# Optimization experiments

Hardware: AMD Instinct MI355X
Metric: run time of the kernel (lower is better)

The kernel has to match this reference:

```python
import jax, jax.numpy as jnp
import numpy as np

N_EXAMPLES = 10  # hardcoded repeat_interleave(10) in the source

def setup_inputs() -> dict:
    key = jax.random.key(0)
    k1, k2, k3, k4 = jax.random.split(key, 4)
    B, L, S, H = 8, 256, 512, 1024
    return {
        "output": jax.random.normal(k1, (B * N_EXAMPLES, L, H), dtype=jnp.float32),
        "context0": jax.random.normal(k2, (B * N_EXAMPLES, L, H), dtype=jnp.float32),
        "context1": jax.random.normal(k3, (B, S, H), dtype=jnp.float32),
        "mask": jnp.zeros((B * N_EXAMPLES, L), dtype=bool),
        "W_out": jax.random.normal(k4, (H, 3 * H), dtype=jnp.float32) * 0.02,
        "b_out": jnp.zeros((H,), dtype=jnp.float32),
    }

def reference(output, context0, context1, mask, W_out, b_out):
    # output, context0: [B*10, L, H]; context1: [B, S, H]
    # NOTE: in the torch source, `attn.data.masked_fill(mask, -inf)` is NOT
    # in-place and its result is discarded, so the mask has no effect on the
    # math. We reproduce that faithfully: `mask` is unused.
    del mask
    set_ctx = jnp.repeat(context1, N_EXAMPLES, axis=0)  # [B*10, S, H]
    # example-attention branch: bmm -> softmax -> bmm
    ex_attn = jax.nn.softmax(jnp.einsum('bld,bsd->bls', output, context0), axis=-1)  # [B*10, L, L]
    # set-attention branch: bmm -> softmax -> bmm
    set_attn = jax.nn.softmax(jnp.einsum('bld,bsd->bls', output, set_ctx), axis=-1)  # [B*10, L, S]
    ex_c = jnp.einsum('bls,bsd->bld', ex_attn, context0)   # [B*10, L, H]
    set_c = jnp.einsum('bls,bsd->bld', set_attn, set_ctx)  # [B*10, L, H]
    all_info = jnp.concatenate([output, ex_c, set_c], axis=-1)  # [B*10, L, 3H]
    out = jnp.tanh(jnp.einsum('blk,hk->blh', all_info, W_out) + b_out)  # [B*10, L, H]
    return (out, ex_attn, set_attn)
```

## Files before the change

### kernel.cpp

```cpp
#include <hip/hip_runtime.h>
#include <stdint.h>
#include <math.h>

typedef unsigned short u16;
typedef __attribute__((ext_vector_type(8))) short short8;
typedef __attribute__((ext_vector_type(4))) float floatx4;

__device__ __forceinline__ u16 f32_to_bf16(float f) {
    union { float f; uint32_t u; } v; v.f = f;
    uint32_t r = v.u + 0x7FFF + ((v.u >> 16) & 1);
    return (u16)(r >> 16);
}
__device__ __forceinline__ float bf16_to_f32(u16 h) {
    union { uint32_t u; float f; } v; v.u = ((uint32_t)h) << 16; return v.f;
}

__device__ __forceinline__ void gl_lds16(const u16* g, u16* l) {
    __builtin_amdgcn_global_load_lds(
        (const __attribute__((address_space(1))) void*)g,
        (__attribute__((address_space(3))) void*)l, 16, 0, 0);
}


__global__ void split_kernel(const float4* __restrict__ x, ushort4* __restrict__ hi,
                             ushort4* __restrict__ lo, long n4) {
    long i = (long)blockIdx.x * blockDim.x + threadIdx.x;
    if (i >= n4) return;
    float4 v = x[i];
    ushort4 h, l;
    h.x = f32_to_bf16(v.x); l.x = f32_to_bf16(v.x - bf16_to_f32(h.x));
    h.y = f32_to_bf16(v.y); l.y = f32_to_bf16(v.y - bf16_to_f32(h.y));
    h.z = f32_to_bf16(v.z); l.z = f32_to_bf16(v.z - bf16_to_f32(h.z));
    h.w = f32_to_bf16(v.w); l.w = f32_to_bf16(v.w - bf16_to_f32(h.w));
    hi[i] = h; lo[i] = l;
}

__global__ void conv_kernel(const float4* __restrict__ x, ushort4* __restrict__ hi, long n4) {
    long i = (long)blockIdx.x * blockDim.x + threadIdx.x;
    if (i >= n4) return;
    float4 v = x[i];
    ushort4 h;
    h.x = f32_to_bf16(v.x); h.y = f32_to_bf16(v.y);
    h.z = f32_to_bf16(v.z); h.w = f32_to_bf16(v.w);
    hi[i] = h;
}

__global__ void transpose_u16(const u16* __restrict__ src, u16* __restrict__ dst,
                              int R, int C) {
    __shared__ u16 tile[32][34];
    long base = (long)blockIdx.z * R * C;
    int c0 = blockIdx.x * 32, r0 = blockIdx.y * 32;
    #pragma unroll
    for (int i = threadIdx.y; i < 32; i += 8)
        tile[i][threadIdx.x] = src[base + (long)(r0 + i) * C + c0 + threadIdx.x];
    __syncthreads();
    #pragma unroll
    for (int i = threadIdx.y; i < 32; i += 8)
        dst[base + (long)(c0 + i) * R + r0 + threadIdx.x] = tile[threadIdx.x][i];
}

template <int VPT>
__global__ void softmax_rows(float* __restrict__ data, u16* __restrict__ outb) {
    int row = blockIdx.x * 4 + (threadIdx.x >> 6);
    int lane = threadIdx.x & 63;
    long base = (long)row * (VPT * 64) + lane;
    float v[VPT];
    #pragma unroll
    for (int i = 0; i < VPT; ++i) v[i] = data[base + i * 64];
    float m = v[0];
    #pragma unroll
    for (int i = 1; i < VPT; ++i) m = fmaxf(m, v[i]);
    #pragma unroll
    for (int off = 32; off > 0; off >>= 1) m = fmaxf(m, __shfl_xor(m, off, 64));
    float s = 0.f;
    #pragma unroll
    for (int i = 0; i < VPT; ++i) { v[i] = __expf(v[i] - m); s += v[i]; }
    #pragma unroll
    for (int off = 32; off > 0; off >>= 1) s += __shfl_xor(s, off, 64);
    float inv = 1.0f / s;
    #pragma unroll
    for (int i = 0; i < VPT; ++i) {
        float r = v[i] * inv;
        data[base + i * 64] = r;
        outb[base + i * 64] = f32_to_bf16(r);
    }
}

struct GemmP {
    const u16* A[3];
    const u16* B[3];
    const u16* B2[3];
    long strideAb, strideBb, strideB2b, strideCb, strideC2b;
    int bdiv, bdiv2, nseg, Kper, kshift, kmask, nt, lda, ldb, ldb2, ldc, ldc2, mode;
    int gx, gy, nx1;
    float* Cf; float* Cf2; u16* Cb; const float* bias;
};

__global__ __launch_bounds__(256) void gemm_bt(GemmP p) {
    __shared__ u16 As[128 * 64];
    __shared__ u16 Bs[128 * 64];
    const int tid  = threadIdx.x;
    const int lane = tid & 63;
    const int wave = tid >> 6;
    const int quad = lane >> 4;
    const int l15  = lane & 15;
    const int wm = (wave & 1) * 64;
    const int wn = (wave >> 1) * 64;

    const int f  = blockIdx.x;
    const int Tx = gridDim.x >> 3;
    const int t  = (f & 7) * Tx + (f >> 3);
    const int n  = t % p.gx;
    const int r  = t / p.gx;
    const int m0 = (r % p.gy) * 128;
    const int bz = r / p.gy;

    const u16* Bsegs[3];
    int ldb, ldc, nn, bdv;
    long bstr, cstr;
    float* Cf;
    if (n < p.nx1) {
        Bsegs[0] = p.B[0]; Bsegs[1] = p.B[1]; Bsegs[2] = p.B[2];
        ldb = p.ldb; ldc = p.ldc; bstr = p.strideBb; cstr = p.strideCb;
        Cf = p.Cf; bdv = p.bdiv; nn = n;
    } else {
        Bsegs[0] = p.B2[0]; Bsegs[1] = p.B2[1]; Bsegs[2] = p.B2[2];
        ldb = p.ldb2; ldc = p.ldc2; bstr = p.strideB2b; cstr = p.strideC2b;
        Cf = p.Cf2; bdv = p.bdiv2; nn = n - p.nx1;
    }
    const int n0 = nn * 128;

    const int stg_r8 = tid >> 3;
    const int stg_c  = ((tid & 7) ^ (stg_r8 & 7)) * 8;
    const int xorl   = l15 & 7;

    floatx4 acc[4][4];
    #pragma unroll
    for (int i = 0; i < 4; ++i)
        #pragma unroll
        for (int j = 0; j < 4; ++j)
            acc[i][j] = (floatx4){0.f, 0.f, 0.f, 0.f};

    const long aoff = (long)bz * p.strideAb + (long)m0 * p.lda;
    const long boff = (long)(bz / bdv) * bstr + (long)n0 * ldb;

    for (int seg = 0; seg < p.nseg; ++seg) {
        const u16* Ag = p.A[seg] + aoff;
        const u16* Bg = Bsegs[seg] + boff;
        for (int k0 = 0; k0 < p.Kper; k0 += 64) {
            __syncthreads();
            #pragma unroll
            for (int i = 0; i < 4; ++i) {
                const int rr = i * 32 + stg_r8;
                gl_lds16(Ag + (long)rr * p.lda + k0 + stg_c, &As[(i * 256 + tid) * 8]);
            }
            #pragma unroll
            for (int i = 0; i < 4; ++i) {
                const int rr = i * 32 + stg_r8;
                gl_lds16(Bg + (long)rr * ldb + k0 + stg_c, &Bs[(i * 256 + tid) * 8]);
            }
            __syncthreads();
            #pragma unroll
            for (int kk = 0; kk < 2; ++kk) {
                const int cs = ((kk * 4 + quad) ^ xorl) * 8;
                short8 af[4], bfr[4];
                #pragma unroll
                for (int i = 0; i < 4; ++i)
                    af[i] = *(const short8*)&As[(wm + i * 16 + l15) * 64 + cs];
                #pragma unroll
                for (int i = 0; i < 4; ++i)
                    bfr[i] = *(const short8*)&Bs[(wn + i * 16 + l15) * 64 + cs];
                #pragma unroll
                for (int mi = 0; mi < 4; ++mi)
                    #pragma unroll
                    for (int ni = 0; ni < 4; ++ni)
                        acc[mi][ni] = __builtin_amdgcn_mfma_f32_16x16x32_bf16(
                            af[mi], bfr[ni], acc[mi][ni], 0, 0, 0);
            }
        }
    }

    const long coff = (long)bz * cstr;
    const int rb = m0 + wm + quad * 4;
    const int cbase = n0 + wn + l15;
    if (p.mode == 2) {
        #pragma unroll
        for (int ni = 0; ni < 4; ++ni) {
            const float bv = p.bias[cbase + ni * 16];
            #pragma unroll
            for (int mi = 0; mi < 4; ++mi)
                #pragma unroll
                for (int j = 0; j < 4; ++j)
                    Cf[coff + (long)(rb + mi * 16 + j) * ldc + cbase + ni * 16] =
                        tanhf(acc[mi][ni][j] + bv);
        }
    } else if (p.mode == 0) {
        #pragma unroll
        for (int ni = 0; ni < 4; ++ni)
            #pragma unroll
            for (int mi = 0; mi < 4; ++mi)
                #pragma unroll
                for (int j = 0; j < 4; ++j)
                    Cf[coff + (long)(rb + mi * 16 + j) * ldc + cbase + ni * 16] =
                        acc[mi][ni][j];
    } else {
        #pragma unroll
        for (int ni = 0; ni < 4; ++ni)
            #pragma unroll
            for (int mi = 0; mi < 4; ++mi)
                #pragma unroll
                for (int j = 0; j < 4; ++j)
                    p.Cb[coff + (long)(rb + mi * 16 + j) * ldc + cbase + ni * 16] =
                        f32_to_bf16(acc[mi][ni][j]);
    }
}

__global__ __launch_bounds__(512, 2) void gemm_bt8(GemmP p) {
    __shared__ u16 As[32768];
    __shared__ u16 Bs[32768];
    const int tid  = threadIdx.x;
    const int lane = tid & 63;
    const int wave = tid >> 6;
    const int quad = lane >> 4;
    const int l15  = lane & 15;
    const int wr   = wave >> 2;
    const int wc   = wave & 3;

    const int f  = blockIdx.x;
    const int Tx = gridDim.x >> 3;
    const int t  = (f & 7) * Tx + (f >> 3);
    const int n  = t % p.gx;
    const int r  = t / p.gx;
    const int m0 = (r % p.gy) * 256;
    const int bz = r / p.gy;

    const u16 *B0, *B1, *B2p;
    int ldb, ldc, nn, bdv;
    long bstr, cstr;
    float* Cf;
    if (n < p.nx1) {
        B0 = p.B[0]; B1 = p.B[1]; B2p = p.B[2];
        ldb = p.ldb; ldc = p.ldc; bstr = p.strideBb; cstr = p.strideCb;
        Cf = p.Cf; bdv = p.bdiv; nn = n;
    } else {
        B0 = p.B2[0]; B1 = p.B2[1]; B2p = p.B2[2];
        ldb = p.ldb2; ldc = p.ldc2; bstr = p.strideB2b; cstr = p.strideC2b;
        Cf = p.Cf2; bdv = p.bdiv2; nn = n - p.nx1;
    }
    const int n0 = nn * 256;

    const long aoff = (long)bz * p.strideAb + (long)m0 * p.lda;
    const long boff = (long)(bz / bdv) * bstr + (long)n0 * ldb;

    const int srow = tid >> 2;
    const int sgc  = ((tid & 3) ^ ((srow >> 1) & 3)) * 8;

    const u16* a0 = p.A[0] + aoff + (long)srow * p.lda + sgc;
    const u16* a1 = p.A[1] + aoff + (long)srow * p.lda + sgc;
    const u16* a2 = p.A[2] + aoff + (long)srow * p.lda + sgc;
    const u16* b0 = B0 + boff + (long)srow * ldb + sgc;
    const u16* b1 = B1 + boff + (long)srow * ldb + sgc;
    const u16* b2 = B2p + boff + (long)srow * ldb + sgc;
    const long aStep128 = (long)128 * p.lda;
    const long bStep128 = (long)128 * ldb;

    const int rA = wr * 128 + l15;
    const u16* pA = As + rA * 32 + ((quad ^ ((rA >> 1) & 3)) * 8);
    const int rB = wc * 64 + l15;
    const u16* pB = Bs + rB * 32 + ((quad ^ ((rB >> 1) & 3)) * 8);

    const int nt = p.nt;

    auto stA = [&](int kt, int kk) {
        if (kt < nt) {
            const int seg = kt >> p.kshift;
            const u16* base = (seg == 0) ? a0 : ((seg == 1) ? a1 : a2);
            const u16* g = base + (((kt & p.kmask) << 6) + kk * 32);
            u16* d = &As[((((kt & 1) << 1) | kk) << 13) + tid * 8];
            gl_lds16(g, d);
            gl_lds16(g + aStep128, d + 4096);
        }
    };
    auto stB = [&](int kt, int kk) {
        if (kt < nt) {
            const int seg = kt >> p.kshift;
            const u16* base = (seg == 0) ? b0 : ((seg == 1) ? b1 : b2);
            const u16* g = base + (((kt & p.kmask) << 6) + kk * 32);
            u16* d = &Bs[((((kt & 1) << 1) | kk) << 13) + tid * 8];
            gl_lds16(g, d);
            gl_lds16(g + bStep128, d + 4096);
        }
    };

    floatx4 acc[8][4];
    #pragma unroll
    for (int i = 0; i < 8; ++i)
        #pragma unroll
        for (int j = 0; j < 4; ++j)
            acc[i][j] = (floatx4){0.f, 0.f, 0.f, 0.f};

    stA(0, 0); stB(0, 0); stA(0, 1); stB(0, 1); stA(1, 0); stB(1, 0);
    asm volatile("s_waitcnt vmcnt(4)" ::: "memory");
    __builtin_amdgcn_s_barrier();

    short8 af[4], bf[4];

#define QPHASE(SO, MH, LOADB, STAGE)                                        \
    {                                                                       \
        _Pragma("unroll")                                                   \
        for (int mi = 0; mi < 4; ++mi)                                      \
            af[mi] = *(const short8*)(pA + (SO) + (MH) * 2048 + mi * 512);  \
        if (LOADB) {                                                        \
            _Pragma("unroll")                                               \
            for (int ni = 0; ni < 4; ++ni)                                  \
                bf[ni] = *(const short8*)(pB + (SO) + ni * 512);            \
        }                                                                   \
        STAGE;                                                              \
        __builtin_amdgcn_s_barrier();                                       \
        asm volatile("s_waitcnt lgkmcnt(0)" ::: "memory");                  \
        __builtin_amdgcn_sched_barrier(0);                                  \
        __builtin_amdgcn_s_setprio(1);                                      \
        _Pragma("unroll")                                                   \
        for (int mi = 0; mi < 4; ++mi)                                      \
            _Pragma("unroll")                                               \
            for (int ni = 0; ni < 4; ++ni)                                  \
                acc[(MH) * 4 + mi][ni] =                                    \
                    __builtin_amdgcn_mfma_f32_16x16x32_bf16(                \
                        af[mi], bf[ni], acc[(MH) * 4 + mi][ni], 0, 0, 0);   \
        __builtin_amdgcn_s_setprio(0);                                      \
        __builtin_amdgcn_sched_barrier(0);                                  \
    }

    for (int kt = 0; kt < nt; ++kt) {
        const int so0 = (kt & 1) << 14;
        const int so1 = so0 + 8192;
        QPHASE(so0, 0, true,  stA(kt + 1, 1));
        __builtin_amdgcn_s_barrier();
        QPHASE(so0, 1, false, stB(kt + 1, 1));
        __builtin_amdgcn_s_barrier();
        QPHASE(so1, 0, true,  stA(kt + 2, 0));
        __builtin_amdgcn_s_barrier();
        QPHASE(so1, 1, false, stB(kt + 2, 0));
        if (kt + 2 < nt) {
            asm volatile("s_waitcnt vmcnt(4)" ::: "memory");
        } else {
            asm volatile("s_waitcnt vmcnt(0)" ::: "memory");
        }
        __builtin_amdgcn_s_barrier();
    }
#undef QPHASE

    const long coff = (long)bz * cstr;
    const int rb = m0 + wr * 128 + quad * 4;
    const int cb = n0 + wc * 64 + l15;
    if (p.mode == 2) {
        #pragma unroll
        for (int ni = 0; ni < 4; ++ni) {
            const float bv = p.bias[cb + ni * 16];
            #pragma unroll
            for (int mi = 0; mi < 8; ++mi)
                #pragma unroll
                for (int j = 0; j < 4; ++j)
                    Cf[coff + (long)(rb + mi * 16 + j) * ldc + cb + ni * 16] =
                        tanhf(acc[mi][ni][j] + bv);
        }
    } else if (p.mode == 0) {
        #pragma unroll
        for (int ni = 0; ni < 4; ++ni)
            #pragma unroll
            for (int mi = 0; mi < 8; ++mi)
                #pragma unroll
                for (int j = 0; j < 4; ++j)
                    Cf[coff + (long)(rb + mi * 16 + j) * ldc + cb + ni * 16] =
                        acc[mi][ni][j];
    } else {
        #pragma unroll
        for (int ni = 0; ni < 4; ++ni)
            #pragma unroll
            for (int mi = 0; mi < 8; ++mi)
                #pragma unroll
                for (int j = 0; j < 4; ++j)
                    p.Cb[coff + (long)(rb + mi * 16 + j) * ldc + cb + ni * 16] =
                        f32_to_bf16(acc[mi][ni][j]);
    }
}

extern "C" void kernel_launch(void* const* d_in, const int* in_sizes, int n_in,
                              void* d_out, int out_size, void* d_ws, size_t ws_size,
                              hipStream_t stream) {
    const int BT = 80, L = 256, S = 512, H = 1024;
    const long NO    = (long)BT * L * H;
    const long NC1   = (long)8 * S * H;
    const long NW    = (long)H * 3 * H;
    const long NEXA  = (long)BT * L * L;
    const long NSETA = (long)BT * L * S;

    const float* X    = (const float*)d_in[0];
    const float* C0   = (const float*)d_in[1];
    const float* C1   = (const float*)d_in[2];
    const float* Wf   = (const float*)d_in[4];
    const float* bias = (const float*)d_in[5];

    float* out  = (float*)d_out;
    float* exa  = out + NO;
    float* seta = exa + NEXA;

    char* wsb = (char*)d_ws;
    size_t off = 0;
    auto alloc = [&](long nbytes) -> void* {
        void* p = (void*)(wsb + off);
        off += ((size_t)nbytes + 255) & ~(size_t)255;
        return p;
    };
    u16* Xhi  = (u16*)alloc(NO * 2);
    u16* Xlo  = (u16*)alloc(NO * 2);
    u16* C0hi = (u16*)alloc(NO * 2);
    u16* C0lo = (u16*)alloc(NO * 2);
    u16* C1hi = (u16*)alloc(NC1 * 2);
    u16* C1lo = (u16*)alloc(NC1 * 2);
    u16* Wb   = (u16*)alloc(NW * 2);
    u16* exab = (u16*)alloc(NEXA * 2);
    u16* setab= (u16*)alloc(NSETA * 2);
    u16* C0T = C0lo;
    u16* C1T = C1lo;
    u16* exc = Xlo;
    u16* setc = C0hi;

    split_kernel<<<(int)(NO / 4 / 256), 256, 0, stream>>>((const float4*)X, (ushort4*)Xhi, (ushort4*)Xlo, NO / 4);
    split_kernel<<<(int)(NO / 4 / 256), 256, 0, stream>>>((const float4*)C0, (ushort4*)C0hi, (ushort4*)C0lo, NO / 4);
    split_kernel<<<(int)(NC1 / 4 / 256), 256, 0, stream>>>((const float4*)C1, (ushort4*)C1hi, (ushort4*)C1lo, NC1 / 4);
    conv_kernel<<<(int)(NW / 4 / 256), 256, 0, stream>>>((const float4*)Wf, (ushort4*)Wb, NW / 4);

    {
        GemmP p{};
        p.A[0] = Xhi;  p.A[1] = Xlo;  p.A[2] = Xhi;
        p.B[0]  = C0hi; p.B[1]  = C0hi; p.B[2]  = C0lo;
        p.B2[0] = C1hi; p.B2[1] = C1hi; p.B2[2] = C1lo;
        p.strideAb = (long)L * H;
        p.strideBb = (long)L * H;  p.strideB2b = (long)S * H;
        p.strideCb = (long)L * L;  p.strideC2b = (long)L * S;
        p.bdiv = 1; p.bdiv2 = 10;
        p.nseg = 3; p.Kper = H; p.lda = H; p.ldb = H; p.ldb2 = H;
        p.ldc = L; p.ldc2 = S; p.mode = 0;
        p.gx = 6; p.gy = 2; p.nx1 = 2;
        p.Cf = exa; p.Cf2 = seta;
        gemm_bt<<<dim3(6 * 2 * BT, 1, 1), 256, 0, stream>>>(p);
    }
    softmax_rows<4><<<BT * L / 4, 256, 0, stream>>>(exa, exab);
    softmax_rows<8><<<BT * L / 4, 256, 0, stream>>>(seta, setab);

    transpose_u16<<<dim3(H / 32, L / 32, BT), dim3(32, 8), 0, stream>>>(C0hi, C0T, L, H);
    transpose_u16<<<dim3(H / 32, S / 32, 8), dim3(32, 8), 0, stream>>>(C1hi, C1T, S, H);

    {
        GemmP p{};
        p.A[0] = exab; p.B[0] = C0T;
        p.strideAb = (long)L * L; p.strideBb = (long)H * L; p.strideCb = (long)L * H;
        p.bdiv = 1; p.kshift = 2; p.kmask = 3; p.nt = 4;
        p.lda = L; p.ldb = L; p.ldc = H; p.mode = 1;
        p.gx = 4; p.gy = 1; p.nx1 = 4;
        p.Cb = exc;
        gemm_bt8<<<dim3(4 * 1 * BT, 1, 1), 512, 0, stream>>>(p);
    }
    {
        GemmP p{};
        p.A[0] = setab; p.B[0] = C1T;
        p.strideAb = (long)L * S; p.strideBb = (long)H * S; p.strideCb = (long)L * H;
        p.bdiv = 10; p.kshift = 3; p.kmask = 7; p.nt = 8;
        p.lda = S; p.ldb = S; p.ldc = H; p.mode = 1;
        p.gx = 4; p.gy = 1; p.nx1 = 4;
        p.Cb = setc;
        gemm_bt8<<<dim3(4 * 1 * BT, 1, 1), 512, 0, stream>>>(p);
    }
    {
        GemmP p{};
        p.A[0] = Xhi; p.A[1] = exc; p.A[2] = setc;
        p.B[0] = Wb;  p.B[1] = Wb + 1024; p.B[2] = Wb + 2048;
        p.strideAb = 0; p.strideBb = 0; p.strideCb = 0;
        p.bdiv = 1; p.nseg = 3; p.Kper = H; p.lda = H; p.ldb = 3 * H; p.ldc = H; p.mode = 2;
        p.gx = 8; p.gy = BT * L / 128; p.nx1 = 8;
        p.Cf = out; p.bias = bias;
        gemm_bt<<<dim3(8 * (BT * L / 128), 1, 1), 256, 0, stream>>>(p);
    }
}
```

Baseline: 865.7 us.

## Run attention-score GEMM on 256x256 pipelined gemm_bt8 kernel with segment-generic B pointers

The first GEMM (scores for both the example and set branches, using a three-segment split-bf16 K loop) moves from the 128x128 single-buffered gemm_bt kernel to the 256x256, 8-wave, double-buffered gemm_bt8 kernel. gemm_bt8 now reads B through the n-dependent Bsegs array, so one launch can serve both output targets, and it computes segment pointers inline instead of precomputing six base pointers. The larger tiles give more data reuse and the staged loads give more overlap, in exchange for fewer blocks (240 instead of 960) and some extra address arithmetic per stage.

```diff
diff --git a/kernel.cpp b/kernel.cpp
--- a/kernel.cpp
+++ b/kernel.cpp
@@ -96,23 +96,23 @@
     float* Cf; float* Cf2; u16* Cb; const float* bias;
 };
 
-__global__ __launch_bounds__(256) void gemm_bt(GemmP p) {
-    __shared__ u16 As[128 * 64];
-    __shared__ u16 Bs[128 * 64];
+__global__ __launch_bounds__(512, 2) void gemm_bt8(GemmP p) {
+    __shared__ u16 As[32768];
+    __shared__ u16 Bs[32768];
     const int tid  = threadIdx.x;
     const int lane = tid & 63;
     const int wave = tid >> 6;
     const int quad = lane >> 4;
     const int l15  = lane & 15;
-    const int wm = (wave & 1) * 64;
-    const int wn = (wave >> 1) * 64;
+    const int wr   = wave >> 2;
+    const int wc   = wave & 3;
 
     const int f  = blockIdx.x;
     const int Tx = gridDim.x >> 3;
     const int t  = (f & 7) * Tx + (f >> 3);
     const int n  = t % p.gx;
     const int r  = t / p.gx;
-    const int m0 = (r % p.gy) * 128;
+    const int m0 = (r % p.gy) * 256;
     const int bz = r / p.gy;
 
     const u16* Bsegs[3];
@@ -128,141 +128,13 @@
         ldb = p.ldb2; ldc = p.ldc2; bstr = p.strideB2b; cstr = p.strideC2b;
         Cf = p.Cf2; bdv = p.bdiv2; nn = n - p.nx1;
     }
-    const int n0 = nn * 128;
-
-    const int stg_r8 = tid >> 3;
-    const int stg_c  = ((tid & 7) ^ (stg_r8 & 7)) * 8;
-    const int xorl   = l15 & 7;
-
-    floatx4 acc[4][4];
-    #pragma unroll
-    for (int i = 0; i < 4; ++i)
-        #pragma unroll
-        for (int j = 0; j < 4; ++j)
-            acc[i][j] = (floatx4){0.f, 0.f, 0.f, 0.f};
+    const int n0 = nn * 256;
 
     const long aoff = (long)bz * p.strideAb + (long)m0 * p.lda;
     const long boff = (long)(bz / bdv) * bstr + (long)n0 * ldb;
 
-    for (int seg = 0; seg < p.nseg; ++seg) {
-        const u16* Ag = p.A[seg] + aoff;
-        const u16* Bg = Bsegs[seg] + boff;
-        for (int k0 = 0; k0 < p.Kper; k0 += 64) {
-            __syncthreads();
-            #pragma unroll
-            for (int i = 0; i < 4; ++i) {
-                const int rr = i * 32 + stg_r8;
-                gl_lds16(Ag + (long)rr * p.lda + k0 + stg_c, &As[(i * 256 + tid) * 8]);
-            }
-            #pragma unroll
-            for (int i = 0; i < 4; ++i) {
-                const int rr = i * 32 + stg_r8;
-                gl_lds16(Bg + (long)rr * ldb + k0 + stg_c, &Bs[(i * 256 + tid) * 8]);
-            }
-            __syncthreads();
-            #pragma unroll
-            for (int kk = 0; kk < 2; ++kk) {
-                const int cs = ((kk * 4 + quad) ^ xorl) * 8;
-                short8 af[4], bfr[4];
-                #pragma unroll
-                for (int i = 0; i < 4; ++i)
-                    af[i] = *(const short8*)&As[(wm + i * 16 + l15) * 64 + cs];
-                #pragma unroll
-                for (int i = 0; i < 4; ++i)
-                    bfr[i] = *(const short8*)&Bs[(wn + i * 16 + l15) * 64 + cs];
-                #pragma unroll
-                for (int mi = 0; mi < 4; ++mi)
-                    #pragma unroll
-                    for (int ni = 0; ni < 4; ++ni)
-                        acc[mi][ni] = __builtin_amdgcn_mfma_f32_16x16x32_bf16(
-                            af[mi], bfr[ni], acc[mi][ni], 0, 0, 0);
-            }
-        }
-    }
-
-    const long coff = (long)bz * cstr;
-    const int rb = m0 + wm + quad * 4;
-    const int cbase = n0 + wn + l15;
-    if (p.mode == 2) {
-        #pragma unroll
-        for (int ni = 0; ni < 4; ++ni) {
-            const float bv = p.bias[cbase + ni * 16];
-            #pragma unroll
-            for (int mi = 0; mi < 4; ++mi)
-                #pragma unroll
-                for (int j = 0; j < 4; ++j)
-                    Cf[coff + (long)(rb + mi * 16 + j) * ldc + cbase + ni * 16] =
-                        tanhf(acc[mi][ni][j] + bv);
-        }
-    } else if (p.mode == 0) {
-        #pragma unroll
-        for (int ni = 0; ni < 4; ++ni)
-            #pragma unroll
-            for (int mi = 0; mi < 4; ++mi)
-                #pragma unroll
-                for (int j = 0; j < 4; ++j)
-                    Cf[coff + (long)(rb + mi * 16 + j) * ldc + cbase + ni * 16] =
-                        acc[mi][ni][j];
-    } else {
-        #pragma unroll
-        for (int ni = 0; ni < 4; ++ni)
-            #pragma unroll
-            for (int mi = 0; mi < 4; ++mi)
-                #pragma unroll
-                for (int j = 0; j < 4; ++j)
-                    p.Cb[coff + (long)(rb + mi * 16 + j) * ldc + cbase + ni * 16] =
-                        f32_to_bf16(acc[mi][ni][j]);
-    }
-}
-
-__global__ __launch_bounds__(512, 2) void gemm_bt8(GemmP p) {
-    __shared__ u16 As[32768];
-    __shared__ u16 Bs[32768];
-    const int tid  = threadIdx.x;
-    const int lane = tid & 63;
-    const int wave = tid >> 6;
-    const int quad = lane >> 4;
-    const int l15  = lane & 15;
-    const int wr   = wave >> 2;
-    const int wc   = wave & 3;
-
-    const int f  = blockIdx.x;
-    const int Tx = gridDim.x >> 3;
-    const int t  = (f & 7) * Tx + (f >> 3);
-    const int n  = t % p.gx;
-    const int r  = t / p.gx;
-    const int m0 = (r % p.gy) * 256;
-    const int bz = r / p.gy;
-
-    const u16 *B0, *B1, *B2p;
-    int ldb, ldc, nn, bdv;
-    long bstr, cstr;
-    float* Cf;
-    if (n < p.nx1) {
-        B0 = p.B[0]; B1 = p.B[1]; B2p = p.B[2];
-        ldb = p.ldb; ldc = p.ldc; bstr = p.strideBb; cstr = p.strideCb;
-        Cf = p.Cf; bdv = p.bdiv; nn = n;
-    } else {
-        B0 = p.B2[0]; B1 = p.B2[1]; B2p = p.B2[2];
-        ldb = p.ldb2; ldc = p.ldc2; bstr = p.strideB2b; cstr = p.strideC2b;
-        Cf = p.Cf2; bdv = p.bdiv2; nn = n - p.nx1;
-    }
-    const int n0 = nn * 256;
-
-    const long aoff = (long)bz * p.strideAb + (long)m0 * p.lda;
-    const long boff = (long)(bz / bdv) * bstr + (long)n0 * ldb;
-
     const int srow = tid >> 2;
     const int sgc  = ((tid & 3) ^ ((srow >> 1) & 3)) * 8;
-
-    const u16* a0 = p.A[0] + aoff + (long)srow * p.lda + sgc;
-    const u16* a1 = p.A[1] + aoff + (long)srow * p.lda + sgc;
-    const u16* a2 = p.A[2] + aoff + (long)srow * p.lda + sgc;
-    const u16* b0 = B0 + boff + (long)srow * ldb + sgc;
-    const u16* b1 = B1 + boff + (long)srow * ldb + sgc;
-    const u16* b2 = B2p + boff + (long)srow * ldb + sgc;
-    const long aStep128 = (long)128 * p.lda;
-    const long bStep128 = (long)128 * ldb;
 
     const int rA = wr * 128 + l15;
     const u16* pA = As + rA * 32 + ((quad ^ ((rA >> 1) & 3)) * 8);
@@ -274,21 +146,21 @@
     auto stA = [&](int kt, int kk) {
         if (kt < nt) {
             const int seg = kt >> p.kshift;
-            const u16* base = (seg == 0) ? a0 : ((seg == 1) ? a1 : a2);
-            const u16* g = base + (((kt & p.kmask) << 6) + kk * 32);
+            const u16* g = p.A[seg] + aoff + (long)srow * p.lda
+                         + (((kt & p.kmask) << 6) + kk * 32 + sgc);
             u16* d = &As[((((kt & 1) << 1) | kk) << 13) + tid * 8];
             gl_lds16(g, d);
-            gl_lds16(g + aStep128, d + 4096);
+            gl_lds16(g + (long)128 * p.lda, d + 4096);
         }
     };
     auto stB = [&](int kt, int kk) {
         if (kt < nt) {
             const int seg = kt >> p.kshift;
-            const u16* base = (seg == 0) ? b0 : ((seg == 1) ? b1 : b2);
-            const u16* g = base + (((kt & p.kmask) << 6) + kk * 32);
+            const u16* g = Bsegs[seg] + boff + (long)srow * ldb
+                         + (((kt & p.kmask) << 6) + kk * 32 + sgc);
             u16* d = &Bs[((((kt & 1) << 1) | kk) << 13) + tid * 8];
             gl_lds16(g, d);
-            gl_lds16(g + bStep128, d + 4096);
+            gl_lds16(g + (long)128 * ldb, d + 4096);
         }
     };
 
@@ -385,6 +257,125 @@
     }
 }
 
+__global__ __launch_bounds__(256) void gemm_bt(GemmP p) {
+    __shared__ u16 As[128 * 64];
+    __shared__ u16 Bs[128 * 64];
+    const int tid  = threadIdx.x;
+    const int lane = tid & 63;
+    const int wave = tid >> 6;
+    const int quad = lane >> 4;
+    const int l15  = lane & 15;
+    const int wm = (wave & 1) * 64;
+    const int wn = (wave >> 1) * 64;
+
+    const int f  = blockIdx.x;
+    const int Tx = gridDim.x >> 3;
+    const int t  = (f & 7) * Tx + (f >> 3);
+    const int n  = t % p.gx;
+    const int r  = t / p.gx;
+    const int m0 = (r % p.gy) * 128;
+    const int bz = r / p.gy;
+
+    const u16* Bsegs[3];
+    int ldb, ldc, nn, bdv;
+    long bstr, cstr;
+    float* Cf;
+    if (n < p.nx1) {
+        Bsegs[0] = p.B[0]; Bsegs[1] = p.B[1]; Bsegs[2] = p.B[2];
+        ldb = p.ldb; ldc = p.ldc; bstr = p.strideBb; cstr = p.strideCb;
+        Cf = p.Cf; bdv = p.bdiv; nn = n;
+    } else {
+        Bsegs[0] = p.B2[0]; Bsegs[1] = p.B2[1]; Bsegs[2] = p.B2[2];
+        ldb = p.ldb2; ldc = p.ldc2; bstr = p.strideB2b; cstr = p.strideC2b;
+        Cf = p.Cf2; bdv = p.bdiv2; nn = n - p.nx1;
+    }
+    const int n0 = nn * 128;
+
+    const int stg_r8 = tid >> 3;
+    const int stg_c  = ((tid & 7) ^ (stg_r8 & 7)) * 8;
+    const int xorl   = l15 & 7;
+
+    floatx4 acc[4][4];
+    #pragma unroll
+    for (int i = 0; i < 4; ++i)
+        #pragma unroll
+        for (int j = 0; j < 4; ++j)
+            acc[i][j] = (floatx4){0.f, 0.f, 0.f, 0.f};
+
+    const long aoff = (long)bz * p.strideAb + (long)m0 * p.lda;
+    const long boff = (long)(bz / bdv) * bstr + (long)n0 * ldb;
+
+    for (int seg = 0; seg < p.nseg; ++seg) {
+        const u16* Ag = p.A[seg] + aoff;
+        const u16* Bg = Bsegs[seg] + boff;
+        for (int k0 = 0; k0 < p.Kper; k0 += 64) {
+            __syncthreads();
+            #pragma unroll
+            for (int i = 0; i < 4; ++i) {
+                const int rr = i * 32 + stg_r8;
+                gl_lds16(Ag + (long)rr * p.lda + k0 + stg_c, &As[(i * 256 + tid) * 8]);
+            }
+            #pragma unroll
+            for (int i = 0; i < 4; ++i) {
+                const int rr = i * 32 + stg_r8;
+                gl_lds16(Bg + (long)rr * ldb + k0 + stg_c, &Bs[(i * 256 + tid) * 8]);
+            }
+            __syncthreads();
+            #pragma unroll
+            for (int kk = 0; kk < 2; ++kk) {
+                const int cs = ((kk * 4 + quad) ^ xorl) * 8;
+                short8 af[4], bfr[4];
+                #pragma unroll
+                for (int i = 0; i < 4; ++i)
+                    af[i] = *(const short8*)&As[(wm + i * 16 + l15) * 64 + cs];
+                #pragma unroll
+                for (int i = 0; i < 4; ++i)
+                    bfr[i] = *(const short8*)&Bs[(wn + i * 16 + l15) * 64 + cs];
+                #pragma unroll
+                for (int mi = 0; mi < 4; ++mi)
+                    #pragma unroll
+                    for (int ni = 0; ni < 4; ++ni)
+                        acc[mi][ni] = __builtin_amdgcn_mfma_f32_16x16x32_bf16(
+                            af[mi], bfr[ni], acc[mi][ni], 0, 0, 0);
+            }
+        }
+    }
+
+    const long coff = (long)bz * cstr;
+    const int rb = m0 + wm + quad * 4;
+    const int cbase = n0 + wn + l15;
+    if (p.mode == 2) {
+        #pragma unroll
+        for (int ni = 0; ni < 4; ++ni) {
+            const float bv = p.bias[cbase + ni * 16];
+            #pragma unroll
+            for (int mi = 0; mi < 4; ++mi)
+                #pragma unroll
+                for (int j = 0; j < 4; ++j)
+                    Cf[coff + (long)(rb + mi * 16 + j) * ldc + cbase + ni * 16] =
+                        tanhf(acc[mi][ni][j] + bv);
+        }
+    } else if (p.mode == 0) {
+        #pragma unroll
+        for (int ni = 0; ni < 4; ++ni)
+            #pragma unroll
+            for (int mi = 0; mi < 4; ++mi)
+                #pragma unroll
+                for (int j = 0; j < 4; ++j)
+                    Cf[coff + (long)(rb + mi * 16 + j) * ldc + cbase + ni * 16] =
+                        acc[mi][ni][j];
+    } else {
+        #pragma unroll
+        for (int ni = 0; ni < 4; ++ni)
+            #pragma unroll
+            for (int mi = 0; mi < 4; ++mi)
+                #pragma unroll
+                for (int j = 0; j < 4; ++j)
+                    p.Cb[coff + (long)(rb + mi * 16 + j) * ldc + cbase + ni * 16] =
+                        f32_to_bf16(acc[mi][ni][j]);
+    }
+}
+
 extern "C" void kernel_launch(void* const* d_in, const int* in_sizes, int n_in,
                               void* d_out, int out_size, void* d_ws, size_t ws_size,
                               hipStream_t stream) {
@@ -440,11 +431,12 @@
         p.strideBb = (long)L * H;  p.strideB2b = (long)S * H;
         p.strideCb = (long)L * L;  p.strideC2b = (long)L * S;
         p.bdiv = 1; p.bdiv2 = 10;
-        p.nseg = 3; p.Kper = H; p.lda = H; p.ldb = H; p.ldb2 = H;
+        p.kshift = 4; p.kmask = 15; p.nt = 48;
+        p.lda = H; p.ldb = H; p.ldb2 = H;
         p.ldc = L; p.ldc2 = S; p.mode = 0;
-        p.gx = 6; p.gy = 2; p.nx1 = 2;
+        p.gx = 3; p.gy = 1; p.nx1 = 1;
         p.Cf = exa; p.Cf2 = seta;
-        gemm_bt<<<dim3(6 * 2 * BT, 1, 1), 256, 0, stream>>>(p);
+        gemm_bt8<<<dim3(3 * 1 * BT, 1, 1), 512, 0, stream>>>(p);
     }
     softmax_rows<4><<<BT * L / 4, 256, 0, stream>>>(exa, exab);
     softmax_rows<8><<<BT * L / 4, 256, 0, stream>>>(seta, setab);
```

Measured after the change: 747.4 us. 1.16x faster.
